# Performance work log

Measured on AMD Instinct MI355X. Metric: run time of the kernel, lower is better.

The kernel has to match this reference:

```python
import jax, jax.numpy as jnp
import numpy as np

B, LR_DIM, G_DIM, K, D, T = 256, 1024, 512, 64, 256, 8
GRID = jnp.linspace(-4.0, 4.0, 41)  # registered buffer in torch module


def _mu_bell(x, c, a_bell, b_bell):
    # generalized bell membership, clamp(a,b) >= 1e-3 as in torch
    a = jnp.maximum(a_bell, 1e-3)
    b = jnp.maximum(b_bell, 1e-3)
    return 1.0 / (1.0 + jnp.abs((x - c) / a) ** (2.0 * b))


def _mu_s(x, a, b):
    eps = 1e-12
    a2 = jnp.minimum(a, b)
    b2 = jnp.maximum(a, b)
    mid = (a2 + b2) * 0.5
    up = 2.0 * ((x - a2) / (b2 - a2 + eps)) ** 2
    dn = 1.0 - 2.0 * ((b2 - x) / (b2 - a2 + eps)) ** 2
    y = jnp.where((x > a2) & (x <= mid), up, jnp.zeros_like(x))
    y = jnp.where((x > mid) & (x <= b2), dn, y)
    return jnp.where(x > b2, jnp.ones_like(x), y)


def _fuzzify(x, a_bell, b_bell):
    # x: (B,d) -> (B,2d)
    xs = 4.0 * jnp.tanh(x / 4.0)
    xb = _mu_bell(xs, 0.0, a_bell, b_bell)
    xS = _mu_s(xs, -1.0, 1.0)
    return jnp.concatenate([xb, xS], axis=-1)


def _defuzzify(rt, a_bell, b_bell):
    # rt: (B,2d) -> centroid (B,d)
    d = rt.shape[1] // 2
    rb, rs = rt[:, :d], rt[:, d:]
    g = GRID[None, None, :]                      # (1,1,G)
    c_b = 4.0 * jnp.tanh(rb)[..., None]          # (B,d,1)
    c_s = 4.0 * jnp.tanh(rs)[..., None]
    mu_b = _mu_bell(g, c_b, a_bell, b_bell)      # (B,d,G)
    a_s = jnp.clip(c_s - 1.0, -4.0, 4.0)
    b_s = jnp.clip(c_s + 1.0, -4.0, 4.0)
    mu_s = _mu_s(g, a_s, b_s)
    cen_b = (g * mu_b).sum(-1) / (mu_b.sum(-1) + 1e-12)
    cen_s = (g * mu_s).sum(-1) / (mu_s.sum(-1) + 1e-12)
    return 0.5 * cen_b + 0.5 * cen_s


def _forward(wsi_lr, genomics, FT, W_lr, b_lr, W_g, b_g, WqI, WqG, WkI, WkG,
             WvI, WvG, mlp_W1, mlp_b1, mlp_W2, mlp_b2, Wf, bf, Wi, bi, Vf, Vi,
             a_bell, b_bell):
    scale = jnp.float32(D) ** 0.5
    lr = wsi_lr @ W_lr + b_lr                    # (B,d)
    g = genomics @ W_g + b_g
    lr_f = _fuzzify(lr, a_bell, b_bell)          # (B,2d)
    g_f = _fuzzify(g, a_bell, b_bell)
    QI = lr_f @ WqI                              # (B,d), loop-invariant
    QG = g_f @ WqG
    Ft0 = jnp.broadcast_to(FT[None], (wsi_lr.shape[0],) + FT.shape)  # (B,K,d)

    def step(Ft, _):
        sI = jnp.einsum('bd,bkd->bk', QI, Ft @ WkI) / scale
        sG = jnp.einsum('bd,bkd->bk', QG, Ft @ WkG) / scale
        rtI = jnp.einsum('bk,bke->be', jax.nn.softmax(sI, axis=-1), Ft @ WvI)  # (B,2d)
        rtG = jnp.einsum('bk,bke->be', jax.nn.softmax(sG, axis=-1), Ft @ WvG)
        r = 0.5 * _defuzzify(rtI, a_bell, b_bell) + 0.5 * _defuzzify(rtG, a_bell, b_bell)
        rb = jnp.broadcast_to(r[:, None, :], Ft.shape)              # (B,K,d)
        x = Ft + rb
        F_tilde = jax.nn.gelu(x @ mlp_W1 + mlp_b1, approximate=False) @ mlp_W2 + mlp_b2 + x
        f_gate = jax.nn.sigmoid(rb @ Wf + bf + jnp.tanh(Ft @ Vf))
        i_gate = jax.nn.sigmoid(rb @ Wi + bi + jnp.tanh(Ft @ Vi))
        Ft_new = f_gate * Ft + i_gate * jnp.tanh(F_tilde)
        return Ft_new, Ft_new

    _, steps = jax.lax.scan(step, Ft0, None, length=T)
    # torch stores step `T-s` result at index s-1: list index 0 holds the LAST
    # computed state, index T-1 the first -> reverse chronological order
    return steps[::-1]  # (T,B,K,d)


def setup_inputs() -> dict:
    key = jax.random.key(0)
    ks = jax.random.split(key, 20)

    def rn(k, shape, scale):
        return jax.random.normal(k, shape, dtype=jnp.float32) * scale

    z = lambda *s: jnp.zeros(s, jnp.float32)
    return dict(
        wsi_lr=rn(ks[0], (B, LR_DIM), 1.0),
        genomics=rn(ks[1], (B, G_DIM), 1.0),
        FT=rn(ks[2], (K, D), 0.02),
        W_lr=rn(ks[3], (LR_DIM, D), LR_DIM ** -0.5), b_lr=z(D),
        W_g=rn(ks[4], (G_DIM, D), G_DIM ** -0.5), b_g=z(D),
        WqI=rn(ks[5], (2 * D, D), (2 * D) ** -0.5),
        WqG=rn(ks[6], (2 * D, D), (2 * D) ** -0.5),
        WkI=rn(ks[7], (D, D), D ** -0.5),
        WkG=rn(ks[8], (D, D), D ** -0.5),
        WvI=rn(ks[9], (D, 2 * D), D ** -0.5),
        WvG=rn(ks[10], (D, 2 * D), D ** -0.5),
        mlp_W1=rn(ks[11], (D, 2 * D), D ** -0.5), mlp_b1=z(2 * D),
        mlp_W2=rn(ks[12], (2 * D, D), (2 * D) ** -0.5), mlp_b2=z(D),
        Wf=rn(ks[13], (D, D), D ** -0.5), bf=z(D),
        Wi=rn(ks[14], (D, D), D ** -0.5), bi=z(D),
        Vf=rn(ks[15], (D, D), D ** -0.5),
        Vi=rn(ks[16], (D, D), D ** -0.5),
        a_bell=jnp.float32(1.0),
        b_bell=jnp.float32(2.0),
    )


def reference(wsi_lr, genomics, FT, W_lr, b_lr, W_g, b_g, WqI, WqG, WkI, WkG,
              WvI, WvG, mlp_W1, mlp_b1, mlp_W2, mlp_b2, Wf, bf, Wi, bi, Vf, Vi,
              a_bell, b_bell):
    return _forward(wsi_lr, genomics, FT, W_lr, b_lr, W_g, b_g, WqI, WqG, WkI,
                    WkG, WvI, WvG, mlp_W1, mlp_b1, mlp_W2, mlp_b2, Wf, bf, Wi,
                    bi, Vf, Vi, a_bell, b_bell)
```

## Files before the change

### kernel.cpp

```cpp
#include <hip/hip_runtime.h>
#include <hip/hip_bf16.h>

#define B_    256
#define K_    64
#define D_    256
#define T_    8
#define NROW  (B_*K_)

typedef short short8v __attribute__((ext_vector_type(8)));
typedef float f32x4  __attribute__((ext_vector_type(4)));

__device__ __forceinline__ float fexp2(float x) { return __builtin_amdgcn_exp2f(x); }
__device__ __forceinline__ float flog2(float x) { return __builtin_amdgcn_logf(x); }

__device__ __forceinline__ float sigmoid_f(float x) {
  return 1.f / (1.f + fexp2(x * -1.4426950408889634f));
}
__device__ __forceinline__ float tanh_fast(float x) {
  float xc = fminf(fmaxf(x, -30.f), 30.f);
  float t = fexp2(xc * 2.8853900817779268f);
  return (t - 1.f) / (t + 1.f);
}
__device__ __forceinline__ float gelu_f(float x) {
  return 0.5f * x * (1.f + erff(x * 0.70710678118654752440f));
}
__device__ __forceinline__ unsigned short f2bf(float x) {
  __hip_bfloat16 h = __float2bfloat16(x);
  return *reinterpret_cast<unsigned short*>(&h);
}
__device__ __forceinline__ float bfss(unsigned short s) {
  return __uint_as_float(((unsigned int)s) << 16);
}
__device__ __forceinline__ float muS_f(float x, float a2, float b2) {
  float mid = 0.5f * (a2 + b2);
  float inv = 1.f / (b2 - a2 + 1e-12f);
  if (x > b2)  return 1.f;
  if (x > mid) { float u = (b2 - x) * inv; return 1.f - 2.f * u * u; }
  if (x > a2)  { float u = (x - a2) * inv; return 2.f * u * u; }
  return 0.f;
}
__device__ __forceinline__ float pow_abs(float z, float e2b) {
  return fexp2(e2b * flog2(fabsf(z)));
}
__device__ __forceinline__ float defuzz_one(float rb_, float rs_, float ab, float bb) {
  float e2b = 2.f * bb;
  float inv_ab = 1.f / ab;
  float cb = 4.f * tanh_fast(rb_);
  float num = 0.f, den = 0.f;
  #pragma unroll
  for (int j = 0; j < 41; ++j) {
    float gj = -4.f + 0.2f * (float)j;
    float mu = 1.f / (1.f + pow_abs((gj - cb) * inv_ab, e2b));
    num += gj * mu; den += mu;
  }
  float cenb = num / (den + 1e-12f);
  float cs = 4.f * tanh_fast(rs_);
  float as_ = fminf(fmaxf(cs - 1.f, -4.f), 4.f);
  float bs_ = fminf(fmaxf(cs + 1.f, -4.f), 4.f);
  num = 0.f; den = 0.f;
  {
    float mid = 0.5f * (as_ + bs_);
    float inv = 1.f / (bs_ - as_ + 1e-12f);
    #pragma unroll
    for (int j = 0; j < 41; ++j) {
      float gj = -4.f + 0.2f * (float)j;
      float mu;
      if (gj > bs_)      mu = 1.f;
      else if (gj > mid) { float u = (bs_ - gj) * inv; mu = 1.f - 2.f * u * u; }
      else if (gj > as_) { float u = (gj - as_) * inv; mu = 2.f * u * u; }
      else               mu = 0.f;
      num += gj * mu; den += mu;
    }
  }
  float cens = num / (den + 1e-12f);
  return 0.5f * cenb + 0.5f * cens;
}

__global__ __launch_bounds__(256) void k_convert(
    const float* __restrict__ W1, const float* __restrict__ Vf, const float* __restrict__ Vi,
    const float* __restrict__ W2, const float* __restrict__ FT,
    const float* __restrict__ WkI, const float* __restrict__ WkG,
    const float* __restrict__ WvI, const float* __restrict__ WvG,
    const float* __restrict__ Wf,  const float* __restrict__ Wi,
    unsigned short* __restrict__ B1t, unsigned short* __restrict__ W2t,
    unsigned short* __restrict__ FTbf,
    float* __restrict__ WkIt, float* __restrict__ WkGt,
    unsigned short* __restrict__ Wv2, unsigned short* __restrict__ WB)
{
  int idx = blockIdx.x * 256 + threadIdx.x;
  if (idx < 262144) {
    int n = idx >> 8, k = idx & 255;
    float v = (n < 512) ? W1[(size_t)k*512 + n]
            : (n < 768) ? Vf[(size_t)k*256 + (n-512)]
                        : Vi[(size_t)k*256 + (n-768)];
    B1t[idx] = f2bf(v);
  } else if (idx < 393216) {
    int j = idx - 262144;
    int n = j >> 9, k = j & 511;
    W2t[j] = f2bf(W2[(size_t)k*256 + n]);
  } else if (idx < 409600) {
    int j = idx - 393216;
    FTbf[j] = f2bf(FT[j]);
  } else if (idx < 475136) {
    int j = idx - 409600;
    int k = j >> 8, n = j & 255;
    WkIt[j] = WkI[(size_t)n*256 + k];
  } else if (idx < 540672) {
    int j = idx - 475136;
    int k = j >> 8, n = j & 255;
    WkGt[j] = WkG[(size_t)n*256 + k];
  } else if (idx < 802816) {
    int j = idx - 540672;
    int d = j >> 10, c = j & 1023;
    float v = (c < 512) ? WvI[(size_t)d*512 + c] : WvG[(size_t)d*512 + (c-512)];
    Wv2[j] = f2bf(v);
  } else if (idx < 1064960) {
    int j = idx - 802816;
    int d = j >> 10, c = j & 1023;
    float v = (c < 512) ? W1[(size_t)d*512 + c]
            : (c < 768) ? Wf[(size_t)d*256 + (c-512)]
                        : Wi[(size_t)d*256 + (c-768)];
    WB[j] = f2bf(v);
  }
}

__global__ __launch_bounds__(256) void k_pre_lin(
    const float* __restrict__ wsi, const float* __restrict__ gen,
    const float* __restrict__ W_lr, const float* __restrict__ b_lr,
    const float* __restrict__ W_g,  const float* __restrict__ b_g,
    const float* __restrict__ a_p,  const float* __restrict__ b_p,
    float* __restrict__ lrf, float* __restrict__ gf)
{
  int g_ix = blockIdx.x;
  int half = g_ix >> 4, tile = g_ix & 15;
  int bx = tile & 3, by = tile >> 2;
  int n0 = bx * 64, m0 = by * 64;
  const float* A    = half ? gen  : wsi;
  const float* Bm   = half ? W_g  : W_lr;
  const float* bias = half ? b_g  : b_lr;
  float* outp       = half ? gf   : lrf;
  int KK            = half ? 512  : 1024;
  float ab = fmaxf(a_p[0], 0.001f), bb = fmaxf(b_p[0], 0.001f);
  float e2b = 2.f * bb, inv_ab = 1.f / ab;

  __shared__ float As[16][64];
  __shared__ float Bs[16][64];
  int tid = threadIdx.x, tx = tid & 15, ty = tid >> 4;
  float acc[4][4] = {};
  int am = tid >> 2, ak = (tid & 3) * 4;
  int bk = tid >> 4, bn = (tid & 15) * 4;
  const float* arow = A + (size_t)(m0 + am) * KK;
  for (int k0 = 0; k0 < KK; k0 += 16) {
    float4 av = *(const float4*)(arow + k0 + ak);
    As[ak+0][am] = av.x; As[ak+1][am] = av.y; As[ak+2][am] = av.z; As[ak+3][am] = av.w;
    *(float4*)&Bs[bk][bn] = *(const float4*)(Bm + (size_t)(k0 + bk) * 256 + n0 + bn);
    __syncthreads();
    #pragma unroll
    for (int kk = 0; kk < 16; ++kk) {
      float a0 = As[kk][ty*4+0], a1 = As[kk][ty*4+1], a2 = As[kk][ty*4+2], a3 = As[kk][ty*4+3];
      float b0 = Bs[kk][tx*4+0], b1 = Bs[kk][tx*4+1], b2 = Bs[kk][tx*4+2], b3 = Bs[kk][tx*4+3];
      acc[0][0]=fmaf(a0,b0,acc[0][0]); acc[0][1]=fmaf(a0,b1,acc[0][1]); acc[0][2]=fmaf(a0,b2,acc[0][2]); acc[0][3]=fmaf(a0,b3,acc[0][3]);
      acc[1][0]=fmaf(a1,b0,acc[1][0]); acc[1][1]=fmaf(a1,b1,acc[1][1]); acc[1][2]=fmaf(a1,b2,acc[1][2]); acc[1][3]=fmaf(a1,b3,acc[1][3]);
      acc[2][0]=fmaf(a2,b0,acc[2][0]); acc[2][1]=fmaf(a2,b1,acc[2][1]); acc[2][2]=fmaf(a2,b2,acc[2][2]); acc[2][3]=fmaf(a2,b3,acc[2][3]);
      acc[3][0]=fmaf(a3,b0,acc[3][0]); acc[3][1]=fmaf(a3,b1,acc[3][1]); acc[3][2]=fmaf(a3,b2,acc[3][2]); acc[3][3]=fmaf(a3,b3,acc[3][3]);
    }
    __syncthreads();
  }
  #pragma unroll
  for (int i = 0; i < 4; ++i) {
    int row = m0 + ty*4 + i;
    #pragma unroll
    for (int j = 0; j < 4; ++j) {
      int col = n0 + tx*4 + j;
      float v = acc[i][j] + bias[col];
      float xs = 4.f * tanh_fast(v * 0.25f);
      outp[(size_t)row*512 + col]       = 1.f / (1.f + pow_abs(xs * inv_ab, e2b));
      outp[(size_t)row*512 + col + 256] = muS_f(xs, -1.f, 1.f);
    }
  }
}

__global__ __launch_bounds__(256) void k_pre_q(
    const float* __restrict__ lrf, const float* __restrict__ gf,
    const float* __restrict__ WqI, const float* __restrict__ WqG,
    float* __restrict__ QI, float* __restrict__ QG)
{
  int g_ix = blockIdx.x;
  int half = g_ix >> 4, tile = g_ix & 15;
  int bx = tile & 3, by = tile >> 2;
  int n0 = bx * 64, m0 = by * 64;
  const float* A  = half ? gf  : lrf;
  const float* Bm = half ? WqG : WqI;
  float* outp     = half ? QG  : QI;

  __shared__ float As[16][64];
  __shared__ float Bs[16][64];
  int tid = threadIdx.x, tx = tid & 15, ty = tid >> 4;
  float acc[4][4] = {};
  int am = tid >> 2, ak = (tid & 3) * 4;
  int bk = tid >> 4, bn = (tid & 15) * 4;
  const float* arow = A + (size_t)(m0 + am) * 512;
  for (int k0 = 0; k0 < 512; k0 += 16) {
    float4 av = *(const float4*)(arow + k0 + ak);
    As[ak+0][am] = av.x; As[ak+1][am] = av.y; As[ak+2][am] = av.z; As[ak+3][am] = av.w;
    *(float4*)&Bs[bk][bn] = *(const float4*)(Bm + (size_t)(k0 + bk) * 256 + n0 + bn);
    __syncthreads();
    #pragma unroll
    for (int kk = 0; kk < 16; ++kk) {
      float a0 = As[kk][ty*4+0], a1 = As[kk][ty*4+1], a2 = As[kk][ty*4+2], a3 = As[kk][ty*4+3];
      float b0 = Bs[kk][tx*4+0], b1 = Bs[kk][tx*4+1], b2 = Bs[kk][tx*4+2], b3 = Bs[kk][tx*4+3];
      acc[0][0]=fmaf(a0,b0,acc[0][0]); acc[0][1]=fmaf(a0,b1,acc[0][1]); acc[0][2]=fmaf(a0,b2,acc[0][2]); acc[0][3]=fmaf(a0,b3,acc[0][3]);
      acc[1][0]=fmaf(a1,b0,acc[1][0]); acc[1][1]=fmaf(a1,b1,acc[1][1]); acc[1][2]=fmaf(a1,b2,acc[1][2]); acc[1][3]=fmaf(a1,b3,acc[1][3]);
      acc[2][0]=fmaf(a2,b0,acc[2][0]); acc[2][1]=fmaf(a2,b1,acc[2][1]); acc[2][2]=fmaf(a2,b2,acc[2][2]); acc[2][3]=fmaf(a2,b3,acc[2][3]);
      acc[3][0]=fmaf(a3,b0,acc[3][0]); acc[3][1]=fmaf(a3,b1,acc[3][1]); acc[3][2]=fmaf(a3,b2,acc[3][2]); acc[3][3]=fmaf(a3,b3,acc[3][3]);
    }
    __syncthreads();
  }
  #pragma unroll
  for (int i = 0; i < 4; ++i) {
    float4 v = make_float4(acc[i][0], acc[i][1], acc[i][2], acc[i][3]);
    *(float4*)(outp + (size_t)(m0 + ty*4 + i) * 256 + n0 + tx*4) = v;
  }
}

__global__ __launch_bounds__(256) void k_pre_qp(
    const float* __restrict__ QI, const float* __restrict__ QG,
    const float* __restrict__ WkIt, const float* __restrict__ WkGt,
    float* __restrict__ qIp, float* __restrict__ qGp)
{
  int g_ix = blockIdx.x;
  int half = g_ix >> 4, tile = g_ix & 15;
  int bx = tile & 3, by = tile >> 2;
  int n0 = bx * 64, m0 = by * 64;
  const float* A  = half ? QG   : QI;
  const float* Bm = half ? WkGt : WkIt;
  float* outp     = half ? qGp  : qIp;

  __shared__ float As[16][64];
  __shared__ float Bs[16][64];
  int tid = threadIdx.x, tx = tid & 15, ty = tid >> 4;
  float acc[4][4] = {};
  int am = tid >> 2, ak = (tid & 3) * 4;
  int bk = tid >> 4, bn = (tid & 15) * 4;
  const float* arow = A + (size_t)(m0 + am) * 256;
  for (int k0 = 0; k0 < 256; k0 += 16) {
    float4 av = *(const float4*)(arow + k0 + ak);
    As[ak+0][am] = av.x; As[ak+1][am] = av.y; As[ak+2][am] = av.z; As[ak+3][am] = av.w;
    *(float4*)&Bs[bk][bn] = *(const float4*)(Bm + (size_t)(k0 + bk) * 256 + n0 + bn);
    __syncthreads();
    #pragma unroll
    for (int kk = 0; kk < 16; ++kk) {
      float a0 = As[kk][ty*4+0], a1 = As[kk][ty*4+1], a2 = As[kk][ty*4+2], a3 = As[kk][ty*4+3];
      float b0 = Bs[kk][tx*4+0], b1 = Bs[kk][tx*4+1], b2 = Bs[kk][tx*4+2], b3 = Bs[kk][tx*4+3];
      acc[0][0]=fmaf(a0,b0,acc[0][0]); acc[0][1]=fmaf(a0,b1,acc[0][1]); acc[0][2]=fmaf(a0,b2,acc[0][2]); acc[0][3]=fmaf(a0,b3,acc[0][3]);
      acc[1][0]=fmaf(a1,b0,acc[1][0]); acc[1][1]=fmaf(a1,b1,acc[1][1]); acc[1][2]=fmaf(a1,b2,acc[1][2]); acc[1][3]=fmaf(a1,b3,acc[1][3]);
      acc[2][0]=fmaf(a2,b0,acc[2][0]); acc[2][1]=fmaf(a2,b1,acc[2][1]); acc[2][2]=fmaf(a2,b2,acc[2][2]); acc[2][3]=fmaf(a2,b3,acc[2][3]);
      acc[3][0]=fmaf(a3,b0,acc[3][0]); acc[3][1]=fmaf(a3,b1,acc[3][1]); acc[3][2]=fmaf(a3,b2,acc[3][2]); acc[3][3]=fmaf(a3,b3,acc[3][3]);
    }
    __syncthreads();
  }
  #pragma unroll
  for (int i = 0; i < 4; ++i) {
    float4 v = make_float4(acc[i][0], acc[i][1], acc[i][2], acc[i][3]);
    *(float4*)(outp + (size_t)(m0 + ty*4 + i) * 256 + n0 + tx*4) = v;
  }
}

__global__ __launch_bounds__(256, 2) void k_step1(
    const unsigned short* __restrict__ Fb_all, int bcast,
    const unsigned short* __restrict__ B1t,
    const float* __restrict__ qIp, const float* __restrict__ qGp,
    const unsigned short* __restrict__ Wv2, const unsigned short* __restrict__ WB,
    const float* __restrict__ a_p, const float* __restrict__ b_p,
    unsigned short* __restrict__ U1, unsigned short* __restrict__ Tf, unsigned short* __restrict__ Ti,
    float* __restrict__ rr, float* __restrict__ rW1,
    float* __restrict__ rWf, float* __restrict__ rWi)
{
  __shared__ __align__(16) char smem[38912];
  int bid = blockIdx.x, tid = threadIdx.x;

  if (bid >= 256) {
    int gb = bid - 256;
    int bx = gb & 7, by = gb >> 3;
    int n0 = bx * 128, m0 = by * 128;
    short* As = (short*)smem;
    short* Bs = As + 128*72;
    int w = tid >> 6, wm = w >> 1, wn = w & 1, lane = tid & 63, lr = lane & 15, lh = lane >> 4;
    f32x4 acc[4][4] = {};
    int srow = tid >> 3, koff = (tid & 7) * 8;
    for (int k0 = 0; k0 < 256; k0 += 64) {
      #pragma unroll
      for (int rnd = 0; rnd < 4; ++rnd) {
        int rrow = rnd * 32 + srow;
        int ar = bcast ? ((m0 + rrow) & 63) : (m0 + rrow);
        *(float4*)&As[rrow*72 + koff] = *(const float4*)&Fb_all[(size_t)ar * 256 + k0 + koff];
        *(float4*)&Bs[rrow*72 + koff] = *(const float4*)&B1t[(size_t)(n0 + rrow) * 256 + k0 + koff];
      }
      __syncthreads();
      #pragma unroll
      for (int ks = 0; ks < 2; ++ks) {
        short8v a[4], b[4];
        #pragma unroll
        for (int m = 0; m < 4; ++m) a[m] = *(const short8v*)&As[(wm*64 + m*16 + lr)*72 + ks*32 + lh*8];
        #pragma unroll
        for (int n = 0; n < 4; ++n) b[n] = *(const short8v*)&Bs[(wn*64 + n*16 + lr)*72 + ks*32 + lh*8];
        #pragma unroll
        for (int m = 0; m < 4; ++m)
          #pragma unroll
          for (int n = 0; n < 4; ++n)
            acc[m][n] = __builtin_amdgcn_mfma_f32_16x16x32_bf16(a[m], b[n], acc[m][n], 0, 0, 0);
      }
      __syncthreads();
    }
    if (bx < 4) {
      #pragma unroll
      for (int n = 0; n < 4; ++n) {
        int col = n0 + wn*64 + n*16 + lr;
        #pragma unroll
        for (int m = 0; m < 4; ++m) {
          int rbase = m0 + wm*64 + m*16 + lh*4;
          #pragma unroll
          for (int r = 0; r < 4; ++r)
            U1[(size_t)(rbase + r) * 512 + col] = f2bf(acc[m][n][r]);
        }
      }
    } else {
      int isI = (bx >= 6);
      unsigned short* outp = isI ? Ti : Tf;
      int cb = isI ? 768 : 512;
      #pragma unroll
      for (int n = 0; n < 4; ++n) {
        int c = n0 + wn*64 + n*16 + lr - cb;
        #pragma unroll
        for (int m = 0; m < 4; ++m) {
          int rbase = m0 + wm*64 + m*16 + lh*4;
          #pragma unroll
          for (int r = 0; r < 4; ++r)
            outp[(size_t)(rbase + r) * 256 + c] = f2bf(tanh_fast(acc[m][n][r]));
        }
      }
    }
    return;
  }

  int b = bid, t = tid;
  short* Fs  = (short*)smem;
  float* qv  = (float*)(smem + 33792);
  float* red = (float*)(smem + 35840);
  float* prl = (float*)(smem + 37888);
  float* ftb = red;

  const unsigned short* Fsrc = bcast ? Fb_all : (Fb_all + (size_t)b * K_ * D_);
  #pragma unroll
  for (int i = 0; i < 8; ++i) {
    int sidx = (i * 256 + t) * 8;
    int row = sidx >> 8, col = sidx & 255;
    *(float4*)&Fs[row * 264 + col] = *(const float4*)&Fsrc[sidx];
  }
  qv[t]       = qIp[(size_t)b*256 + t];
  qv[256 + t] = qGp[(size_t)b*256 + t];
  __syncthreads();

  {
    int k = t & 63, part = t >> 6;
    const unsigned int* frow = (const unsigned int*)&Fs[k * 264 + part * 64];
    const float* q0 = qv + part * 64;
    const float* q1 = qv + 256 + part * 64;
    float s0 = 0.f, s1 = 0.f;
    #pragma unroll
    for (int d2 = 0; d2 < 32; ++d2) {
      unsigned int pr = frow[d2];
      float f0 = __uint_as_float(pr << 16);
      float f1 = __uint_as_float(pr & 0xffff0000u);
      s0 = fmaf(f1, q0[2*d2+1], fmaf(f0, q0[2*d2], s0));
      s1 = fmaf(f1, q1[2*d2+1], fmaf(f0, q1[2*d2], s1));
    }
    red[t] = s0; red[256 + t] = s1;
  }
  __syncthreads();
  if (t < 128) {
    int which = t >> 6, kk = t & 63;
    const float* rp = red + which * 256;
    float s = (rp[kk] + rp[64+kk] + rp[128+kk] + rp[192+kk]) * (1.f/16.f);
    float m = s;
    for (int off = 32; off; off >>= 1) m = fmaxf(m, __shfl_xor(m, off, 64));
    float e = fexp2((s - m) * 1.4426950408889634f);
    float sum = e;
    for (int off = 32; off; off >>= 1) sum += __shfl_xor(sum, off, 64);
    prl[which * 64 + kk] = e / sum;
  }
  __syncthreads();
  {
    float f0 = 0.f, f1 = 0.f;
    #pragma unroll 8
    for (int kk = 0; kk < 64; ++kk) {
      float fv = bfss((unsigned short)Fs[kk * 264 + t]);
      f0 = fmaf(prl[kk],      fv, f0);
      f1 = fmaf(prl[64 + kk], fv, f1);
    }
    __syncthreads();
    ftb[t] = f0; ftb[256 + t] = f1;
  }
  __syncthreads();
  float aI0 = 0.f, aI1 = 0.f, aG0 = 0.f, aG1 = 0.f;
  #pragma unroll 4
  for (int d = 0; d < 256; ++d) {
    float fI = ftb[d], fG = ftb[256 + d];
    const unsigned short* wr = Wv2 + ((size_t)d << 10);
    aI0 = fmaf(fI, bfss(wr[t]),       aI0);
    aI1 = fmaf(fI, bfss(wr[t + 256]), aI1);
    aG0 = fmaf(fG, bfss(wr[512 + t]), aG0);
    aG1 = fmaf(fG, bfss(wr[768 + t]), aG1);
  }
  {
    float ab = fmaxf(a_p[0], 0.001f), bb = fmaxf(b_p[0], 0.001f);
    float rI = defuzz_one(aI0, aI1, ab, bb);
    float rG = defuzz_one(aG0, aG1, ab, bb);
    float rv = 0.5f * rI + 0.5f * rG;
    __syncthreads();
    prl[t] = rv;
    rr[(size_t)b*256 + t] = rv;
  }
  __syncthreads();
  {
    float w0 = 0.f, w1 = 0.f, wf = 0.f, wi = 0.f;
    #pragma unroll 4
    for (int d = 0; d < 256; ++d) {
      float rv = prl[d];
      const unsigned short* wr = WB + ((size_t)d << 10);
      w0 = fmaf(rv, bfss(wr[t]),       w0);
      w1 = fmaf(rv, bfss(wr[t + 256]), w1);
      wf = fmaf(rv, bfss(wr[512 + t]), wf);
      wi = fmaf(rv, bfss(wr[768 + t]), wi);
    }
    rW1[(size_t)b*512 + t]       = w0;
    rW1[(size_t)b*512 + t + 256] = w1;
    rWf[(size_t)b*256 + t] = wf;
    rWi[(size_t)b*256 + t] = wi;
  }
}

__global__ __launch_bounds__(256) void mfma_gemm2(
    const unsigned short* __restrict__ U1, const unsigned short* __restrict__ W2t,
    const float* __restrict__ b1, const float* __restrict__ b2,
    const float* __restrict__ rW1,
    const float* __restrict__ Fprev, const float* __restrict__ FT, int bcast,
    const float* __restrict__ rr,
    const float* __restrict__ rWf, const float* __restrict__ bfv,
    const float* __restrict__ rWi, const float* __restrict__ biv,
    const unsigned short* __restrict__ Tf, const unsigned short* __restrict__ Ti,
    float* __restrict__ Fout, unsigned short* __restrict__ Fbf)
{
  int bx = blockIdx.x & 1, by = blockIdx.x >> 1;
  int n0 = bx * 128, m0 = by * 64;
  __shared__ __align__(16) short As[64][72];
  __shared__ __align__(16) short Bs[128][72];
  int tid = threadIdx.x;
  int w = tid >> 6, lane = tid & 63, lr = lane & 15, lh = lane >> 4;
  f32x4 acc[4][2] = {};
  int srow = tid >> 3, koff = (tid & 7) * 8;
  const float* rwrow = rW1 + (size_t)by * 512;

  for (int k0 = 0; k0 < 512; k0 += 64) {
    float add_[8];
    #pragma unroll
    for (int q = 0; q < 8; ++q) add_[q] = rwrow[k0 + koff + q] + b1[k0 + koff + q];
    #pragma unroll
    for (int rnd = 0; rnd < 2; ++rnd) {
      int rrow = rnd * 32 + srow;
      int row = m0 + rrow;
      uint4 u = *(const uint4*)&U1[(size_t)row * 512 + k0 + koff];
      unsigned int uu[4] = {u.x, u.y, u.z, u.w};
      unsigned int pk[4];
      #pragma unroll
      for (int q = 0; q < 4; ++q) {
        float lo = __uint_as_float(uu[q] << 16)         + add_[2*q];
        float hi = __uint_as_float(uu[q] & 0xffff0000u) + add_[2*q+1];
        pk[q] = (((unsigned int)f2bf(gelu_f(hi))) << 16) | f2bf(gelu_f(lo));
      }
      uint4 pv; pv.x = pk[0]; pv.y = pk[1]; pv.z = pk[2]; pv.w = pk[3];
      *(uint4*)&As[rrow][koff] = pv;
    }
    #pragma unroll
    for (int rnd = 0; rnd < 4; ++rnd) {
      int rrow = rnd * 32 + srow;
      *(float4*)&Bs[rrow][koff] = *(const float4*)&W2t[(size_t)(n0 + rrow) * 512 + k0 + koff];
    }
    __syncthreads();
    #pragma unroll
    for (int ks = 0; ks < 2; ++ks) {
      short8v a[4], b[2];
      #pragma unroll
      for (int m = 0; m < 4; ++m) a[m] = *(const short8v*)&As[m*16 + lr][ks*32 + lh*8];
      #pragma unroll
      for (int n = 0; n < 2; ++n) b[n] = *(const short8v*)&Bs[w*32 + n*16 + lr][ks*32 + lh*8];
      #pragma unroll
      for (int m = 0; m < 4; ++m)
        #pragma unroll
        for (int n = 0; n < 2; ++n)
          acc[m][n] = __builtin_amdgcn_mfma_f32_16x16x32_bf16(a[m], b[n], acc[m][n], 0, 0, 0);
    }
    __syncthreads();
  }

  int bnum = by;
  const float* rp = rr + (size_t)bnum * 256;
  #pragma unroll
  for (int n = 0; n < 2; ++n) {
    int col = n0 + w*32 + n*16 + lr;
    float b2c = b2[col], rv = rp[col];
    float gf_ = rWf[(size_t)bnum*256 + col] + bfv[col];
    float gi_ = rWi[(size_t)bnum*256 + col] + biv[col];
    #pragma unroll
    for (int m = 0; m < 4; ++m) {
      int rbase = m0 + m*16 + lh*4;
      #pragma unroll
      for (int r = 0; r < 4; ++r) {
        int row = rbase + r;
        float Ftv = bcast ? FT[(size_t)(row & 63) * 256 + col]
                          : Fprev[(size_t)row * 256 + col];
        float ftld = acc[m][n][r] + b2c + Ftv + rv;
        float fg = sigmoid_f(gf_ + bfss(Tf[(size_t)row * 256 + col]));
        float ig = sigmoid_f(gi_ + bfss(Ti[(size_t)row * 256 + col]));
        float ov = fg * Ftv + ig * tanh_fast(ftld);
        Fout[(size_t)row * 256 + col] = ov;
        Fbf[(size_t)row * 256 + col] = f2bf(ov);
      }
    }
  }
}

extern "C" void kernel_launch(void* const* d_in, const int* in_sizes, int n_in,
                              void* d_out, int out_size, void* d_ws, size_t ws_size,
                              hipStream_t stream)
{
  (void)in_sizes; (void)n_in; (void)out_size; (void)ws_size;
  const float* wsi  = (const float*)d_in[0];
  const float* gen  = (const float*)d_in[1];
  const float* FT   = (const float*)d_in[2];
  const float* W_lr = (const float*)d_in[3];
  const float* b_lr = (const float*)d_in[4];
  const float* W_g  = (const float*)d_in[5];
  const float* b_g  = (const float*)d_in[6];
  const float* WqI  = (const float*)d_in[7];
  const float* WqG  = (const float*)d_in[8];
  const float* WkI  = (const float*)d_in[9];
  const float* WkG  = (const float*)d_in[10];
  const float* WvI  = (const float*)d_in[11];
  const float* WvG  = (const float*)d_in[12];
  const float* W1   = (const float*)d_in[13];
  const float* b1   = (const float*)d_in[14];
  const float* W2   = (const float*)d_in[15];
  const float* b2   = (const float*)d_in[16];
  const float* Wf   = (const float*)d_in[17];
  const float* bf   = (const float*)d_in[18];
  const float* Wi   = (const float*)d_in[19];
  const float* bi   = (const float*)d_in[20];
  const float* Vf   = (const float*)d_in[21];
  const float* Vi   = (const float*)d_in[22];
  const float* a_p  = (const float*)d_in[23];
  const float* b_p  = (const float*)d_in[24];

  float* out = (float*)d_out;
  float* ws  = (float*)d_ws;
  float* rr    = ws;
  float* rW1   = rr    + 65536;
  float* rWf   = rW1   + 131072;
  float* rWi   = rWf   + 65536;
  float* qIp   = rWi   + 65536;
  float* qGp   = qIp   + 65536;
  float* lrf   = qGp   + 65536;
  float* gf    = lrf   + 131072;
  float* QI    = gf    + 131072;
  float* QG    = QI    + 65536;
  float* WkIt  = QG    + 65536;
  float* WkGt  = WkIt  + 65536;
  unsigned short* U1   = (unsigned short*)(WkGt + 65536);
  unsigned short* Tfb  = U1   + 8388608;
  unsigned short* Tib  = Tfb  + 4194304;
  unsigned short* Fbf  = Tib  + 4194304;
  unsigned short* FTbf = Fbf  + 4194304;
  unsigned short* B1t  = FTbf + 16384;
  unsigned short* W2t  = B1t  + 262144;
  unsigned short* Wv2  = W2t  + 131072;
  unsigned short* WB   = Wv2  + 262144;

  k_convert<<<4160, 256, 0, stream>>>(W1, Vf, Vi, W2, FT, WkI, WkG, WvI, WvG, Wf, Wi,
                                      B1t, W2t, FTbf, WkIt, WkGt, Wv2, WB);
  k_pre_lin<<<32, 256, 0, stream>>>(wsi, gen, W_lr, b_lr, W_g, b_g, a_p, b_p, lrf, gf);
  k_pre_q<<<32, 256, 0, stream>>>(lrf, gf, WqI, WqG, QI, QG);
  k_pre_qp<<<32, 256, 0, stream>>>(QI, QG, WkIt, WkGt, qIp, qGp);

  const float* Fcur = nullptr;
  int bcast = 1;
  for (int st = 0; st < T_; ++st) {
    float* Fnext = out + (size_t)(7 - st) * NROW * D_;
    k_step1<<<1280, 256, 0, stream>>>(bcast ? FTbf : Fbf, bcast, B1t, qIp, qGp,
                                      Wv2, WB, a_p, b_p,
                                      U1, Tfb, Tib, rr, rW1, rWf, rWi);
    mfma_gemm2<<<512, 256, 0, stream>>>(U1, W2t, b1, b2, rW1, Fcur, FT, bcast, rr,
                                        rWf, bf, rWi, bi, Tfb, Tib, Fnext, Fbf);
    Fcur = Fnext;
    bcast = 0;
  }
}
```

Measured before the change: 1.077 ms.

## Fuse all recurrent steps into one persistent per-batch scan kernel

Replaces the per-step pair of launches (k_step1 plus mfma_gemm2, sixteen launches in total) with a single kernel, k_scan, that runs one 512-thread block per batch element across all eight steps. The state F stays resident in LDS as bf16. The first GEMM, GELU and second GEMM are chained chunk by chunk through LDS, so the large U1 intermediate is never written to or read from global memory. Each block now re-streams the B1t and W2t weights from cache every step, with no overlap between loads and MFMA work. Gate values are still round-tripped through global Gf/Gi buffers.

```diff
diff --git a/kernel.cpp b/kernel.cpp
--- a/kernel.cpp
+++ b/kernel.cpp
@@ -266,267 +266,210 @@
   }
 }
 
-__global__ __launch_bounds__(256, 2) void k_step1(
-    const unsigned short* __restrict__ Fb_all, int bcast,
-    const unsigned short* __restrict__ B1t,
+__global__ __launch_bounds__(512) void k_scan(
+    const unsigned short* __restrict__ FTbf, const float* __restrict__ FTf,
     const float* __restrict__ qIp, const float* __restrict__ qGp,
     const unsigned short* __restrict__ Wv2, const unsigned short* __restrict__ WB,
+    const float* __restrict__ b1, const float* __restrict__ bfv,
+    const float* __restrict__ biv, const float* __restrict__ b2,
+    const unsigned short* __restrict__ B1t, const unsigned short* __restrict__ W2t,
     const float* __restrict__ a_p, const float* __restrict__ b_p,
-    unsigned short* __restrict__ U1, unsigned short* __restrict__ Tf, unsigned short* __restrict__ Ti,
-    float* __restrict__ rr, float* __restrict__ rW1,
-    float* __restrict__ rWf, float* __restrict__ rWi)
+    unsigned short* __restrict__ Gf, unsigned short* __restrict__ Gi,
+    float* __restrict__ out)
 {
-  __shared__ __align__(16) char smem[38912];
-  int bid = blockIdx.x, tid = threadIdx.x;
-
-  if (bid >= 256) {
-    int gb = bid - 256;
-    int bx = gb & 7, by = gb >> 3;
-    int n0 = bx * 128, m0 = by * 128;
-    short* As = (short*)smem;
-    short* Bs = As + 128*72;
-    int w = tid >> 6, wm = w >> 1, wn = w & 1, lane = tid & 63, lr = lane & 15, lh = lane >> 4;
-    f32x4 acc[4][4] = {};
-    int srow = tid >> 3, koff = (tid & 7) * 8;
-    for (int k0 = 0; k0 < 256; k0 += 64) {
-      #pragma unroll
-      for (int rnd = 0; rnd < 4; ++rnd) {
-        int rrow = rnd * 32 + srow;
-        int ar = bcast ? ((m0 + rrow) & 63) : (m0 + rrow);
-        *(float4*)&As[rrow*72 + koff] = *(const float4*)&Fb_all[(size_t)ar * 256 + k0 + koff];
-        *(float4*)&Bs[rrow*72 + koff] = *(const float4*)&B1t[(size_t)(n0 + rrow) * 256 + k0 + koff];
+  __shared__ __align__(16) short Fs[64*264];
+  __shared__ __align__(16) short Bstage[64*264];
+  __shared__ __align__(16) short Wstage[256*72];
+  __shared__ __align__(16) short A2ch[64*72];
+  __shared__ float qv[512];
+  __shared__ float red[512];
+  __shared__ float prl[128];
+  __shared__ float ftb[512];
+  __shared__ float rL[256];
+  __shared__ float rWall[1024];
+
+  int b = blockIdx.x, tid = threadIdx.x;
+  int w = tid >> 6, lane = tid & 63, lr = lane & 15, lh = lane >> 4;
+  int rg = w & 3, cg = w >> 2;
+  float ab = fmaxf(a_p[0], 0.001f), bb = fmaxf(b_p[0], 0.001f);
+
+  #pragma unroll
+  for (int p = 0; p < 4; ++p) {
+    int idx = (p*512 + tid) * 8;
+    int row = idx >> 8, col = idx & 255;
+    *(float4*)&Fs[row*264 + col] = *(const float4*)&FTbf[idx];
+  }
+  qv[tid] = (tid < 256) ? qIp[(size_t)b*256 + tid] : qGp[(size_t)b*256 + tid - 256];
+  __syncthreads();
+
+  const float* Fprev = nullptr;
+  for (int st = 0; st < T_; ++st) {
+    float* Fout = out + (size_t)(7 - st) * NROW * 256;
+
+    {
+      int which = tid >> 8, tt = tid & 255, k = tt & 63, part = tt >> 6;
+      const unsigned int* frow = (const unsigned int*)&Fs[k*264 + part*64];
+      const float* q0 = qv + which*256 + part*64;
+      float s0 = 0.f;
+      #pragma unroll
+      for (int d2 = 0; d2 < 32; ++d2) {
+        unsigned int pr = frow[d2];
+        float f0 = __uint_as_float(pr << 16);
+        float f1 = __uint_as_float(pr & 0xffff0000u);
+        s0 = fmaf(f1, q0[2*d2+1], fmaf(f0, q0[2*d2], s0));
+      }
+      red[which*256 + tt] = s0;
+    }
+    __syncthreads();
+    if (tid < 128) {
+      int which = tid >> 6, kk = tid & 63;
+      const float* rp = red + which*256;
+      float s = (rp[kk] + rp[64+kk] + rp[128+kk] + rp[192+kk]) * (1.f/16.f);
+      float m = s;
+      for (int off = 32; off; off >>= 1) m = fmaxf(m, __shfl_xor(m, off, 64));
+      float e = fexp2((s - m) * 1.4426950408889634f);
+      float sum = e;
+      for (int off = 32; off; off >>= 1) sum += __shfl_xor(sum, off, 64);
+      prl[which*64 + kk] = e / sum;
+    }
+    __syncthreads();
+    {
+      int which = tid >> 8, tt = tid & 255;
+      const float* pp = prl + which*64;
+      float f0 = 0.f;
+      #pragma unroll 8
+      for (int kk = 0; kk < 64; ++kk)
+        f0 = fmaf(pp[kk], bfss((unsigned short)Fs[kk*264 + tt]), f0);
+      ftb[which*256 + tt] = f0;
+    }
+    __syncthreads();
+    {
+      int half = tid >> 8, tt = tid & 255;
+      const float* fb = ftb + half*256;
+      const unsigned short* wv = Wv2 + half*512 + tt;
+      float a0 = 0.f, a1 = 0.f;
+      #pragma unroll 4
+      for (int d = 0; d < 256; ++d) {
+        float fv = fb[d];
+        a0 = fmaf(fv, bfss(wv[(size_t)d*1024]),       a0);
+        a1 = fmaf(fv, bfss(wv[(size_t)d*1024 + 256]), a1);
+      }
+      red[half*256 + tt] = defuzz_one(a0, a1, ab, bb);
+    }
+    __syncthreads();
+    if (tid < 256) rL[tid] = 0.5f * (red[tid] + red[256 + tid]);
+    __syncthreads();
+    {
+      float w0 = 0.f, w1 = 0.f;
+      const unsigned short* wb0 = WB + tid;
+      #pragma unroll 4
+      for (int d = 0; d < 256; ++d) {
+        float rv = rL[d];
+        w0 = fmaf(rv, bfss(wb0[(size_t)d*1024]),       w0);
+        w1 = fmaf(rv, bfss(wb0[(size_t)d*1024 + 512]), w1);
+      }
+      rWall[tid]       = w0 + b1[tid];
+      rWall[512 + tid] = w1 + ((tid < 256) ? bfv[tid] : biv[tid - 256]);
+    }
+    __syncthreads();
+
+    for (int c = 8; c < 16; ++c) {
+      #pragma unroll
+      for (int p = 0; p < 4; ++p) {
+        int idx = (p*512 + tid) * 8;
+        int row = idx >> 8, col = idx & 255;
+        *(float4*)&Bstage[row*264 + col] = *(const float4*)&B1t[(size_t)c*16384 + idx];
       }
       __syncthreads();
       #pragma unroll
-      for (int ks = 0; ks < 2; ++ks) {
-        short8v a[4], b[4];
+      for (int f = 0; f < 2; ++f) {
+        f32x4 acc = {0.f,0.f,0.f,0.f};
+        int nb = cg*32 + f*16;
         #pragma unroll
-        for (int m = 0; m < 4; ++m) a[m] = *(const short8v*)&As[(wm*64 + m*16 + lr)*72 + ks*32 + lh*8];
+        for (int ks = 0; ks < 8; ++ks) {
+          short8v av = *(const short8v*)&Fs[(rg*16 + lr)*264 + ks*32 + lh*8];
+          short8v bv = *(const short8v*)&Bstage[(nb + lr)*264 + ks*32 + lh*8];
+          acc = __builtin_amdgcn_mfma_f32_16x16x32_bf16(av, bv, acc, 0, 0, 0);
+        }
+        int gc = c*64 + nb + lr;
+        float add = rWall[gc];
+        int cc = gc - 512;
         #pragma unroll
-        for (int n = 0; n < 4; ++n) b[n] = *(const short8v*)&Bs[(wn*64 + n*16 + lr)*72 + ks*32 + lh*8];
+        for (int r = 0; r < 4; ++r) {
+          int row = b*64 + rg*16 + lh*4 + r;
+          unsigned short val = f2bf(sigmoid_f(add + tanh_fast(acc[r])));
+          if (cc < 256) Gf[(size_t)row*256 + cc]       = val;
+          else          Gi[(size_t)row*256 + cc - 256] = val;
+        }
+      }
+      __syncthreads();
+    }
+
+    f32x4 O[8];
+    #pragma unroll
+    for (int nn = 0; nn < 8; ++nn) { O[nn][0]=0.f; O[nn][1]=0.f; O[nn][2]=0.f; O[nn][3]=0.f; }
+    for (int c = 0; c < 8; ++c) {
+      #pragma unroll
+      for (int p = 0; p < 4; ++p) {
+        int idx = (p*512 + tid) * 8;
+        int row = idx >> 8, col = idx & 255;
+        *(float4*)&Bstage[row*264 + col] = *(const float4*)&B1t[(size_t)c*16384 + idx];
+      }
+      #pragma unroll
+      for (int p = 0; p < 4; ++p) {
+        int idx = (p*512 + tid) * 8;
+        int n = idx >> 6, kk = idx & 63;
+        *(float4*)&Wstage[n*72 + kk] = *(const float4*)&W2t[(size_t)n*512 + c*64 + kk];
+      }
+      __syncthreads();
+      #pragma unroll
+      for (int f = 0; f < 2; ++f) {
+        f32x4 acc = {0.f,0.f,0.f,0.f};
+        int nb = cg*32 + f*16;
         #pragma unroll
-        for (int m = 0; m < 4; ++m)
-          #pragma unroll
-          for (int n = 0; n < 4; ++n)
-            acc[m][n] = __builtin_amdgcn_mfma_f32_16x16x32_bf16(a[m], b[n], acc[m][n], 0, 0, 0);
+        for (int ks = 0; ks < 8; ++ks) {
+          short8v av = *(const short8v*)&Fs[(rg*16 + lr)*264 + ks*32 + lh*8];
+          short8v bv = *(const short8v*)&Bstage[(nb + lr)*264 + ks*32 + lh*8];
+          acc = __builtin_amdgcn_mfma_f32_16x16x32_bf16(av, bv, acc, 0, 0, 0);
+        }
+        int gc = c*64 + nb + lr;
+        float add = rWall[gc];
+        #pragma unroll
+        for (int r = 0; r < 4; ++r)
+          A2ch[(rg*16 + lh*4 + r)*72 + nb + lr] = f2bf(gelu_f(acc[r] + add));
       }
       __syncthreads();
-    }
-    if (bx < 4) {
-      #pragma unroll
-      for (int n = 0; n < 4; ++n) {
-        int col = n0 + wn*64 + n*16 + lr;
+      #pragma unroll
+      for (int ks2 = 0; ks2 < 2; ++ks2) {
+        short8v av = *(const short8v*)&A2ch[(rg*16 + lr)*72 + ks2*32 + lh*8];
         #pragma unroll
-        for (int m = 0; m < 4; ++m) {
-          int rbase = m0 + wm*64 + m*16 + lh*4;
-          #pragma unroll
-          for (int r = 0; r < 4; ++r)
-            U1[(size_t)(rbase + r) * 512 + col] = f2bf(acc[m][n][r]);
+        for (int nn = 0; nn < 8; ++nn) {
+          short8v bv = *(const short8v*)&Wstage[(cg*128 + nn*16 + lr)*72 + ks2*32 + lh*8];
+          O[nn] = __builtin_amdgcn_mfma_f32_16x16x32_bf16(av, bv, O[nn], 0, 0, 0);
         }
       }
-    } else {
-      int isI = (bx >= 6);
-      unsigned short* outp = isI ? Ti : Tf;
-      int cb = isI ? 768 : 512;
-      #pragma unroll
-      for (int n = 0; n < 4; ++n) {
-        int c = n0 + wn*64 + n*16 + lr - cb;
-        #pragma unroll
-        for (int m = 0; m < 4; ++m) {
-          int rbase = m0 + wm*64 + m*16 + lh*4;
-          #pragma unroll
-          for (int r = 0; r < 4; ++r)
-            outp[(size_t)(rbase + r) * 256 + c] = f2bf(tanh_fast(acc[m][n][r]));
-        }
-      }
-    }
-    return;
-  }
-
-  int b = bid, t = tid;
-  short* Fs  = (short*)smem;
-  float* qv  = (float*)(smem + 33792);
-  float* red = (float*)(smem + 35840);
-  float* prl = (float*)(smem + 37888);
-  float* ftb = red;
-
-  const unsigned short* Fsrc = bcast ? Fb_all : (Fb_all + (size_t)b * K_ * D_);
-  #pragma unroll
-  for (int i = 0; i < 8; ++i) {
-    int sidx = (i * 256 + t) * 8;
-    int row = sidx >> 8, col = sidx & 255;
-    *(float4*)&Fs[row * 264 + col] = *(const float4*)&Fsrc[sidx];
-  }
-  qv[t]       = qIp[(size_t)b*256 + t];
-  qv[256 + t] = qGp[(size_t)b*256 + t];
-  __syncthreads();
-
-  {
-    int k = t & 63, part = t >> 6;
-    const unsigned int* frow = (const unsigned int*)&Fs[k * 264 + part * 64];
-    const float* q0 = qv + part * 64;
-    const float* q1 = qv + 256 + part * 64;
-    float s0 = 0.f, s1 = 0.f;
-    #pragma unroll
-    for (int d2 = 0; d2 < 32; ++d2) {
-      unsigned int pr = frow[d2];
-      float f0 = __uint_as_float(pr << 16);
-      float f1 = __uint_as_float(pr & 0xffff0000u);
-      s0 = fmaf(f1, q0[2*d2+1], fmaf(f0, q0[2*d2], s0));
-      s1 = fmaf(f1, q1[2*d2+1], fmaf(f0, q1[2*d2], s1));
-    }
-    red[t] = s0; red[256 + t] = s1;
-  }
-  __syncthreads();
-  if (t < 128) {
-    int which = t >> 6, kk = t & 63;
-    const float* rp = red + which * 256;
-    float s = (rp[kk] + rp[64+kk] + rp[128+kk] + rp[192+kk]) * (1.f/16.f);
-    float m = s;
-    for (int off = 32; off; off >>= 1) m = fmaxf(m, __shfl_xor(m, off, 64));
-    float e = fexp2((s - m) * 1.4426950408889634f);
-    float sum = e;
-    for (int off = 32; off; off >>= 1) sum += __shfl_xor(sum, off, 64);
-    prl[which * 64 + kk] = e / sum;
-  }
-  __syncthreads();
-  {
-    float f0 = 0.f, f1 = 0.f;
-    #pragma unroll 8
-    for (int kk = 0; kk < 64; ++kk) {
-      float fv = bfss((unsigned short)Fs[kk * 264 + t]);
-      f0 = fmaf(prl[kk],      fv, f0);
-      f1 = fmaf(prl[64 + kk], fv, f1);
-    }
-    __syncthreads();
-    ftb[t] = f0; ftb[256 + t] = f1;
-  }
-  __syncthreads();
-  float aI0 = 0.f, aI1 = 0.f, aG0 = 0.f, aG1 = 0.f;
-  #pragma unroll 4
-  for (int d = 0; d < 256; ++d) {
-    float fI = ftb[d], fG = ftb[256 + d];
-    const unsigned short* wr = Wv2 + ((size_t)d << 10);
-    aI0 = fmaf(fI, bfss(wr[t]),       aI0);
-    aI1 = fmaf(fI, bfss(wr[t + 256]), aI1);
-    aG0 = fmaf(fG, bfss(wr[512 + t]), aG0);
-    aG1 = fmaf(fG, bfss(wr[768 + t]), aG1);
-  }
-  {
-    float ab = fmaxf(a_p[0], 0.001f), bb = fmaxf(b_p[0], 0.001f);
-    float rI = defuzz_one(aI0, aI1, ab, bb);
-    float rG = defuzz_one(aG0, aG1, ab, bb);
-    float rv = 0.5f * rI + 0.5f * rG;
-    __syncthreads();
-    prl[t] = rv;
-    rr[(size_t)b*256 + t] = rv;
-  }
-  __syncthreads();
-  {
-    float w0 = 0.f, w1 = 0.f, wf = 0.f, wi = 0.f;
-    #pragma unroll 4
-    for (int d = 0; d < 256; ++d) {
-      float rv = prl[d];
-      const unsigned short* wr = WB + ((size_t)d << 10);
-      w0 = fmaf(rv, bfss(wr[t]),       w0);
-      w1 = fmaf(rv, bfss(wr[t + 256]), w1);
-      wf = fmaf(rv, bfss(wr[512 + t]), wf);
-      wi = fmaf(rv, bfss(wr[768 + t]), wi);
-    }
-    rW1[(size_t)b*512 + t]       = w0;
-    rW1[(size_t)b*512 + t + 256] = w1;
-    rWf[(size_t)b*256 + t] = wf;
-    rWi[(size_t)b*256 + t] = wi;
-  }
-}
-
-__global__ __launch_bounds__(256) void mfma_gemm2(
-    const unsigned short* __restrict__ U1, const unsigned short* __restrict__ W2t,
-    const float* __restrict__ b1, const float* __restrict__ b2,
-    const float* __restrict__ rW1,
-    const float* __restrict__ Fprev, const float* __restrict__ FT, int bcast,
-    const float* __restrict__ rr,
-    const float* __restrict__ rWf, const float* __restrict__ bfv,
-    const float* __restrict__ rWi, const float* __restrict__ biv,
-    const unsigned short* __restrict__ Tf, const unsigned short* __restrict__ Ti,
-    float* __restrict__ Fout, unsigned short* __restrict__ Fbf)
-{
-  int bx = blockIdx.x & 1, by = blockIdx.x >> 1;
-  int n0 = bx * 128, m0 = by * 64;
-  __shared__ __align__(16) short As[64][72];
-  __shared__ __align__(16) short Bs[128][72];
-  int tid = threadIdx.x;
-  int w = tid >> 6, lane = tid & 63, lr = lane & 15, lh = lane >> 4;
-  f32x4 acc[4][2] = {};
-  int srow = tid >> 3, koff = (tid & 7) * 8;
-  const float* rwrow = rW1 + (size_t)by * 512;
-
-  for (int k0 = 0; k0 < 512; k0 += 64) {
-    float add_[8];
-    #pragma unroll
-    for (int q = 0; q < 8; ++q) add_[q] = rwrow[k0 + koff + q] + b1[k0 + koff + q];
-    #pragma unroll
-    for (int rnd = 0; rnd < 2; ++rnd) {
-      int rrow = rnd * 32 + srow;
-      int row = m0 + rrow;
-      uint4 u = *(const uint4*)&U1[(size_t)row * 512 + k0 + koff];
-      unsigned int uu[4] = {u.x, u.y, u.z, u.w};
-      unsigned int pk[4];
-      #pragma unroll
-      for (int q = 0; q < 4; ++q) {
-        float lo = __uint_as_float(uu[q] << 16)         + add_[2*q];
-        float hi = __uint_as_float(uu[q] & 0xffff0000u) + add_[2*q+1];
-        pk[q] = (((unsigned int)f2bf(gelu_f(hi))) << 16) | f2bf(gelu_f(lo));
-      }
-      uint4 pv; pv.x = pk[0]; pv.y = pk[1]; pv.z = pk[2]; pv.w = pk[3];
-      *(uint4*)&As[rrow][koff] = pv;
-    }
-    #pragma unroll
-    for (int rnd = 0; rnd < 4; ++rnd) {
-      int rrow = rnd * 32 + srow;
-      *(float4*)&Bs[rrow][koff] = *(const float4*)&W2t[(size_t)(n0 + rrow) * 512 + k0 + koff];
-    }
-    __syncthreads();
-    #pragma unroll
-    for (int ks = 0; ks < 2; ++ks) {
-      short8v a[4], b[2];
-      #pragma unroll
-      for (int m = 0; m < 4; ++m) a[m] = *(const short8v*)&As[m*16 + lr][ks*32 + lh*8];
-      #pragma unroll
-      for (int n = 0; n < 2; ++n) b[n] = *(const short8v*)&Bs[w*32 + n*16 + lr][ks*32 + lh*8];
-      #pragma unroll
-      for (int m = 0; m < 4; ++m)
-        #pragma unroll
-        for (int n = 0; n < 2; ++n)
-          acc[m][n] = __builtin_amdgcn_mfma_f32_16x16x32_bf16(a[m], b[n], acc[m][n], 0, 0, 0);
-    }
-    __syncthreads();
-  }
-
-  int bnum = by;
-  const float* rp = rr + (size_t)bnum * 256;
-  #pragma unroll
-  for (int n = 0; n < 2; ++n) {
-    int col = n0 + w*32 + n*16 + lr;
-    float b2c = b2[col], rv = rp[col];
-    float gf_ = rWf[(size_t)bnum*256 + col] + bfv[col];
-    float gi_ = rWi[(size_t)bnum*256 + col] + biv[col];
-    #pragma unroll
-    for (int m = 0; m < 4; ++m) {
-      int rbase = m0 + m*16 + lh*4;
+      __syncthreads();
+    }
+
+    #pragma unroll
+    for (int nn = 0; nn < 8; ++nn) {
+      int col = cg*128 + nn*16 + lr;
+      float b2c = b2[col], rv = rL[col];
       #pragma unroll
       for (int r = 0; r < 4; ++r) {
-        int row = rbase + r;
-        float Ftv = bcast ? FT[(size_t)(row & 63) * 256 + col]
-                          : Fprev[(size_t)row * 256 + col];
-        float ftld = acc[m][n][r] + b2c + Ftv + rv;
-        float fg = sigmoid_f(gf_ + bfss(Tf[(size_t)row * 256 + col]));
-        float ig = sigmoid_f(gi_ + bfss(Ti[(size_t)row * 256 + col]));
+        int rowl = rg*16 + lh*4 + r;
+        int row = b*64 + rowl;
+        float Ftv = (st == 0) ? FTf[rowl*256 + col] : Fprev[(size_t)row*256 + col];
+        float ftld = O[nn][r] + b2c + Ftv + rv;
+        float fg = bfss(Gf[(size_t)row*256 + col]);
+        float ig = bfss(Gi[(size_t)row*256 + col]);
         float ov = fg * Ftv + ig * tanh_fast(ftld);
-        Fout[(size_t)row * 256 + col] = ov;
-        Fbf[(size_t)row * 256 + col] = f2bf(ov);
-      }
-    }
+        Fout[(size_t)row*256 + col] = ov;
+        Fs[rowl*264 + col] = f2bf(ov);
+      }
+    }
+    Fprev = Fout;
+    __syncthreads();
   }
 }
 
@@ -563,11 +506,7 @@
 
   float* out = (float*)d_out;
   float* ws  = (float*)d_ws;
-  float* rr    = ws;
-  float* rW1   = rr    + 65536;
-  float* rWf   = rW1   + 131072;
-  float* rWi   = rWf   + 65536;
-  float* qIp   = rWi   + 65536;
+  float* qIp   = ws;
   float* qGp   = qIp   + 65536;
   float* lrf   = qGp   + 65536;
   float* gf    = lrf   + 131072;
@@ -575,11 +514,9 @@
   float* QG    = QI    + 65536;
   float* WkIt  = QG    + 65536;
   float* WkGt  = WkIt  + 65536;
-  unsigned short* U1   = (unsigned short*)(WkGt + 65536);
-  unsigned short* Tfb  = U1   + 8388608;
-  unsigned short* Tib  = Tfb  + 4194304;
-  unsigned short* Fbf  = Tib  + 4194304;
-  unsigned short* FTbf = Fbf  + 4194304;
+  unsigned short* Gfb  = (unsigned short*)(WkGt + 65536);
+  unsigned short* Gib  = Gfb  + 4194304;
+  unsigned short* FTbf = Gib  + 4194304;
   unsigned short* B1t  = FTbf + 16384;
   unsigned short* W2t  = B1t  + 262144;
   unsigned short* Wv2  = W2t  + 131072;
@@ -591,16 +528,7 @@
   k_pre_q<<<32, 256, 0, stream>>>(lrf, gf, WqI, WqG, QI, QG);
   k_pre_qp<<<32, 256, 0, stream>>>(QI, QG, WkIt, WkGt, qIp, qGp);
 
-  const float* Fcur = nullptr;
-  int bcast = 1;
-  for (int st = 0; st < T_; ++st) {
-    float* Fnext = out + (size_t)(7 - st) * NROW * D_;
-    k_step1<<<1280, 256, 0, stream>>>(bcast ? FTbf : Fbf, bcast, B1t, qIp, qGp,
-                                      Wv2, WB, a_p, b_p,
-                                      U1, Tfb, Tib, rr, rW1, rWf, rWi);
-    mfma_gemm2<<<512, 256, 0, stream>>>(U1, W2t, b1, b2, rW1, Fcur, FT, bcast, rr,
-                                        rWf, bf, rWi, bi, Tfb, Tib, Fnext, Fbf);
-    Fcur = Fnext;
-    bcast = 0;
-  }
-}
+  k_scan<<<256, 512, 0, stream>>>(FTbf, FT, qIp, qGp, Wv2, WB,
+                                  b1, bf, bi, b2, B1t, W2t, a_p, b_p,
+                                  Gfb, Gib, out);
+}
```

Result: faster. 870.3 us (-19.2%).
